# Kernel tuning notes

Hardware: AMD Instinct MI355X
Metric: run time of the kernel (lower is better)

Reference implementation:

```python
import jax, jax.numpy as jnp
import numpy as np

NEG = 1e12  # matches torch code's -1e12 masking constant


def _rope_sincos(seq_len, dim, dtype):
    # SinusoidalPositionEmbedding with merge_mode='zero':
    # emb[n, i] pairs -> reshape to [n, dim] as [sin0, cos0, sin1, cos1, ...]
    pos = jnp.arange(seq_len, dtype=jnp.float32)
    inv = jnp.power(10000.0, -2.0 * jnp.arange(dim // 2, dtype=jnp.float32) / dim)
    ang = pos[:, None] * inv[None, :]            # [n, d/2]
    sin, cos = jnp.sin(ang), jnp.cos(ang)
    # cos_pos = pos[..., 1::2].repeat_interleave(2) == repeat(cos, 2)
    cos_pos = jnp.repeat(cos, 2, axis=-1).astype(dtype)  # [n, d]
    sin_pos = jnp.repeat(sin, 2, axis=-1).astype(dtype)  # [n, d]
    return sin_pos, cos_pos


def _rotate_half(x):
    # stack([-x[..., 1::2], x[..., ::2]], -1).reshape(x.shape)
    x2 = jnp.stack([-x[..., 1::2], x[..., ::2]], axis=-1)
    return x2.reshape(x.shape)


def setup_inputs() -> dict:
    key = jax.random.key(0)
    k1, k2, k3 = jax.random.split(key, 3)
    B, N, H = 8, 1024, 768
    heads, head_size = 12, 64
    inputs = jax.random.normal(k1, (B, N, H), dtype=jnp.float32)
    mask = jnp.ones((B, N), dtype=jnp.float32)
    W = jax.random.normal(k2, (H, heads * head_size * 2), dtype=jnp.float32) * (H ** -0.5)
    b = jnp.zeros((heads * head_size * 2,), dtype=jnp.float32)
    return {"inputs": inputs, "mask": mask, "W": W, "b": b}


def reference(inputs, mask, W, b):
    heads, head_size = 12, 64
    B, N, _ = inputs.shape
    x = inputs @ W + b                              # [B, N, heads*head_size*2]
    x = x.reshape(B, N, heads, 2 * head_size)       # split+stack over heads
    qw, kw = x[..., :head_size], x[..., head_size:]  # [B, N, heads, d]

    sin_pos, cos_pos = _rope_sincos(N, head_size, inputs.dtype)
    sin_pos = sin_pos[None, :, None, :]             # [1, N, 1, d]
    cos_pos = cos_pos[None, :, None, :]
    qw = qw * cos_pos + _rotate_half(qw) * sin_pos
    kw = kw * cos_pos + _rotate_half(kw) * sin_pos

    logits = jnp.einsum('bmhd,bnhd->bhmn', qw, kw)  # [B, heads, N, N]

    m1 = mask[:, None, :, None]                     # mask rows (axis ndim-2)
    m2 = mask[:, None, None, :]                     # mask cols (axis ndim-1)
    logits = logits * m1 + (-NEG) * (1.0 - m1)
    logits = logits * m2 + (-NEG) * (1.0 - m2)
    tril = jnp.tril(jnp.ones((N, N), dtype=logits.dtype), k=-1)
    logits = logits - tril * NEG                    # forbid end < start
    return logits / (head_size ** 0.5)
```

## Files before the change

### kernel.cpp

```cpp
#include <hip/hip_runtime.h>
#include <stdint.h>

#define NEGC 1000000000000.0f

using f32x4  = __attribute__((ext_vector_type(4))) float;
using short8 = __attribute__((ext_vector_type(8))) short;

typedef __attribute__((address_space(3))) uint32_t* lds_ptr_t;
typedef const __attribute__((address_space(1))) uint32_t* gptr_t;

__device__ __forceinline__ void gload_lds16(const void* g, const void* l) {
  __builtin_amdgcn_global_load_lds((gptr_t)g, (lds_ptr_t)l, 16, 0, 0);
}

__device__ __forceinline__ unsigned short f2bf(float f) {
  union { float f; uint32_t u; } v; v.f = f;
  uint32_t u = v.u;
  return (unsigned short)((u + 0x7fffu + ((u >> 16) & 1u)) >> 16);
}

__global__ void k_sincos(float* __restrict__ s, float* __restrict__ c) {
  int idx = blockIdx.x * 256 + threadIdx.x;
  int m = idx >> 5, i = idx & 31;
  float inv = expf(-(float)i * (9.210340371976184f / 32.0f));
  float ang = (float)m * inv;
  s[idx] = sinf(ang);
  c[idx] = cosf(ang);
}

__global__ void k_cvt(const float* __restrict__ in, unsigned short* __restrict__ out, int n4) {
  int idx = blockIdx.x * blockDim.x + threadIdx.x;
  if (idx < n4) {
    float4 v = ((const float4*)in)[idx];
    ushort4 o;
    o.x = f2bf(v.x); o.y = f2bf(v.y); o.z = f2bf(v.z); o.w = f2bf(v.w);
    ((ushort4*)out)[idx] = o;
  }
}

__global__ void k_transW(const float* __restrict__ W, unsigned short* __restrict__ Wt) {
  __shared__ float tile[64][65];
  int kb = blockIdx.x;
  int nb = blockIdx.y;
  int t = threadIdx.x;
  int c = t & 63, r0 = t >> 6;
#pragma unroll
  for (int p = 0; p < 16; ++p) {
    int r = r0 + p * 4;
    tile[r][c] = W[(size_t)(kb * 64 + r) * 1536 + nb * 64 + c];
  }
  __syncthreads();
#pragma unroll
  for (int p = 0; p < 16; ++p) {
    int n = r0 + p * 4;
    Wt[(size_t)(nb * 64 + n) * 768 + kb * 64 + c] = f2bf(tile[c][n]);
  }
}

__global__ __launch_bounds__(256) void k_gemm1(
    const unsigned short* __restrict__ A,
    const unsigned short* __restrict__ Bt,
    const float* __restrict__ bias,
    const float* __restrict__ ssin, const float* __restrict__ scos,
    unsigned short* __restrict__ qb, unsigned short* __restrict__ kb) {
  __shared__ __align__(16) unsigned short As[128 * 64];
  __shared__ __align__(16) unsigned short Bs[128 * 64];
  const int tid = threadIdx.x;
  const int wave = tid >> 6, lane = tid & 63;
  const int wm = wave >> 1, wn = wave & 1;
  const int m0 = blockIdx.x * 128;
  const int h  = blockIdx.y;
  const int j0 = h * 128;
  const int lr = lane >> 3, kc = lane & 7;

  f32x4 acc[4][4] = {};

  for (int kt = 0; kt < 12; ++kt) {
    const int k0 = kt * 64;
#pragma unroll
    for (int i = 0; i < 4; ++i) {
      int row = i * 32 + wave * 8 + lr;
      int gk = k0 + ((kc ^ (row & 7)) << 3);
      gload_lds16(&A[(size_t)(m0 + row) * 768 + gk], &As[(i * 32 + wave * 8) * 64]);
    }
#pragma unroll
    for (int i = 0; i < 4; ++i) {
      int row = i * 32 + wave * 8 + lr;
      int gk = k0 + ((kc ^ (row & 7)) << 3);
      gload_lds16(&Bt[(size_t)(j0 + row) * 768 + gk], &Bs[(i * 32 + wave * 8) * 64]);
    }
    asm volatile("s_waitcnt vmcnt(0)" ::: "memory");
    __syncthreads();
#pragma unroll
    for (int kh = 0; kh < 2; ++kh) {
      short8 af[4], bfr[4];
#pragma unroll
      for (int mt = 0; mt < 4; ++mt) {
        int row = wm * 64 + mt * 16 + (lane & 15);
        int cs = (kh * 4 + (lane >> 4)) ^ (row & 7);
        af[mt] = *(const short8*)&As[row * 64 + cs * 8];
      }
#pragma unroll
      for (int nt = 0; nt < 4; ++nt) {
        int row = wn * 64 + nt * 16 + (lane & 15);
        int cs = (kh * 4 + (lane >> 4)) ^ (row & 7);
        bfr[nt] = *(const short8*)&Bs[row * 64 + cs * 8];
      }
#pragma unroll
      for (int mt = 0; mt < 4; ++mt)
#pragma unroll
        for (int nt = 0; nt < 4; ++nt)
          acc[mt][nt] = __builtin_amdgcn_mfma_f32_16x16x32_bf16(af[mt], bfr[nt], acc[mt][nt], 0, 0, 0);
    }
    __syncthreads();
  }

  const int col = lane & 15, rquad = lane >> 4;
  unsigned short* dst = (wn == 0) ? qb : kb;
#pragma unroll
  for (int nt = 0; nt < 4; ++nt) {
    const int d = nt * 16 + col;
    const float bv = bias[j0 + wn * 64 + d];
    const int ifr = d >> 1;
    const float sgn = (d & 1) ? 1.0f : -1.0f;
#pragma unroll
    for (int mt = 0; mt < 4; ++mt) {
#pragma unroll
      for (int j = 0; j < 4; ++j) {
        int mg = m0 + wm * 64 + mt * 16 + rquad * 4 + j;
        int ms = mg & 1023, bi = mg >> 10;
        float v = acc[mt][nt][j] + bv;
        float p = __shfl_xor(v, 1, 64);
        float s = ssin[ms * 32 + ifr], cv = scos[ms * 32 + ifr];
        float r = v * cv + sgn * p * s;
        dst[(size_t)((bi * 12 + h) * 1024 + ms) * 64 + d] = f2bf(r);
      }
    }
  }
}

__global__ __launch_bounds__(256) void k_gemm2(
    const unsigned short* __restrict__ qb, const unsigned short* __restrict__ kbuf,
    const float* __restrict__ mask, float* __restrict__ out) {
  __shared__ __align__(16) unsigned short Qs[128 * 64];
  __shared__ __align__(16) unsigned short Ks[128 * 64];
  const int tid = threadIdx.x;
  const int wave = tid >> 6, lane = tid & 63;
  const int wm = wave >> 1, wn = wave & 1;
  const int bh = blockIdx.y;
  const int tm = blockIdx.x >> 3, tn = blockIdx.x & 7;
  const int b = bh / 12;
  const int lr = lane >> 3, kc = lane & 7;

  const unsigned short* qbase = qb   + (size_t)bh * (1024 * 64);
  const unsigned short* kbase = kbuf + (size_t)bh * (1024 * 64);

#pragma unroll
  for (int i = 0; i < 4; ++i) {
    int row = i * 32 + wave * 8 + lr;
    int gk = (kc ^ (row & 7)) << 3;
    gload_lds16(&qbase[(size_t)(tm * 128 + row) * 64 + gk], &Qs[(i * 32 + wave * 8) * 64]);
  }
#pragma unroll
  for (int i = 0; i < 4; ++i) {
    int row = i * 32 + wave * 8 + lr;
    int gk = (kc ^ (row & 7)) << 3;
    gload_lds16(&kbase[(size_t)(tn * 128 + row) * 64 + gk], &Ks[(i * 32 + wave * 8) * 64]);
  }
  asm volatile("s_waitcnt vmcnt(0)" ::: "memory");
  __syncthreads();

  f32x4 acc[4][4] = {};
#pragma unroll
  for (int kh = 0; kh < 2; ++kh) {
    short8 af[4], bfr[4];
#pragma unroll
    for (int mt = 0; mt < 4; ++mt) {
      int row = wm * 64 + mt * 16 + (lane & 15);
      int cs = (kh * 4 + (lane >> 4)) ^ (row & 7);
      af[mt] = *(const short8*)&Qs[row * 64 + cs * 8];
    }
#pragma unroll
    for (int nt = 0; nt < 4; ++nt) {
      int row = wn * 64 + nt * 16 + (lane & 15);
      int cs = (kh * 4 + (lane >> 4)) ^ (row & 7);
      bfr[nt] = *(const short8*)&Ks[row * 64 + cs * 8];
    }
#pragma unroll
    for (int mt = 0; mt < 4; ++mt)
#pragma unroll
      for (int nt = 0; nt < 4; ++nt)
        acc[mt][nt] = __builtin_amdgcn_mfma_f32_16x16x32_bf16(af[mt], bfr[nt], acc[mt][nt], 0, 0, 0);
  }

  float* obase = out + (size_t)bh * (1024 * 1024);
  const int col = lane & 15, rquad = lane >> 4;
  float m2v[4]; int ngv[4];
#pragma unroll
  for (int nt = 0; nt < 4; ++nt) {
    ngv[nt] = tn * 128 + wn * 64 + nt * 16 + col;
    m2v[nt] = mask[b * 1024 + ngv[nt]];
  }
#pragma unroll
  for (int mt = 0; mt < 4; ++mt) {
#pragma unroll
    for (int j = 0; j < 4; ++j) {
      int mg = tm * 128 + wm * 64 + mt * 16 + rquad * 4 + j;
      float m1 = mask[b * 1024 + mg];
      float* orow = obase + (size_t)mg * 1024;
#pragma unroll
      for (int nt = 0; nt < 4; ++nt) {
        float v = acc[mt][nt][j];
        v = v * m1 - NEGC * (1.0f - m1);
        v = v * m2v[nt] - NEGC * (1.0f - m2v[nt]);
        if (ngv[nt] < mg) v -= NEGC;
        orow[ngv[nt]] = v * 0.125f;
      }
    }
  }
}

extern "C" void kernel_launch(void* const* d_in, const int* in_sizes, int n_in,
                              void* d_out, int out_size, void* d_ws, size_t ws_size,
                              hipStream_t stream) {
  const float* inputs = (const float*)d_in[0];
  const float* mask   = (const float*)d_in[1];
  const float* W      = (const float*)d_in[2];
  const float* bias   = (const float*)d_in[3];
  float* out = (float*)d_out;
  char* ws = (char*)d_ws;

  float* ssin = (float*)(ws);
  float* scos = (float*)(ws + 131072);
  unsigned short* inA = (unsigned short*)(ws + 262144);
  unsigned short* Wt  = (unsigned short*)(ws + 262144 + 12582912);
  unsigned short* qb  = (unsigned short*)(ws + 262144 + 12582912 + 2359296);
  unsigned short* kb  = (unsigned short*)(ws + 262144 + 12582912 + 2359296 + 12582912);

  hipLaunchKernelGGL(k_sincos, dim3(128), dim3(256), 0, stream, ssin, scos);
  hipLaunchKernelGGL(k_cvt, dim3(6144), dim3(256), 0, stream, inputs, inA, 1572864);
  hipLaunchKernelGGL(k_transW, dim3(12, 24), dim3(256), 0, stream, W, Wt);
  hipLaunchKernelGGL(k_gemm1, dim3(64, 12), dim3(256), 0, stream,
                     inA, Wt, bias, ssin, scos, qb, kb);
  hipLaunchKernelGGL(k_gemm2, dim3(64, 96), dim3(256), 0, stream, qb, kb, mask, out);
}
```

Before: 140.2 us.

## Fuse prep kernels into one launch and remap GEMM blocks for XCD locality

Merges the bf16 input conversion, the W transpose and the sin/cos table kernels into a single launch that branches on block index. This removes two launches and their inter-kernel gaps. Both GEMM kernels now use a 1D grid whose block index is remapped so that blocks dispatched to the same XCD share M-tiles (gemm1) or batch-head slices (gemm2), aiming for better L2 reuse per XCD. The remapping assumes round-robin dispatch of blocks across 8 XCDs. The fused prep kernel also allocates the transpose tile in shared memory for every block, including those that never use it.

```diff
diff --git a/kernel.cpp b/kernel.cpp
--- a/kernel.cpp
+++ b/kernel.cpp
@@ -19,41 +19,40 @@
   return (unsigned short)((u + 0x7fffu + ((u >> 16) & 1u)) >> 16);
 }
 
-__global__ void k_sincos(float* __restrict__ s, float* __restrict__ c) {
-  int idx = blockIdx.x * 256 + threadIdx.x;
-  int m = idx >> 5, i = idx & 31;
-  float inv = expf(-(float)i * (9.210340371976184f / 32.0f));
-  float ang = (float)m * inv;
-  s[idx] = sinf(ang);
-  c[idx] = cosf(ang);
-}
-
-__global__ void k_cvt(const float* __restrict__ in, unsigned short* __restrict__ out, int n4) {
-  int idx = blockIdx.x * blockDim.x + threadIdx.x;
-  if (idx < n4) {
+__global__ __launch_bounds__(256) void k_prep(
+    const float* __restrict__ in, unsigned short* __restrict__ inb,
+    const float* __restrict__ W, unsigned short* __restrict__ Wt,
+    float* __restrict__ ssin, float* __restrict__ scos) {
+  __shared__ float tile[64][65];
+  const int bx = blockIdx.x, t = threadIdx.x;
+  if (bx < 6144) {
+    int idx = bx * 256 + t;
     float4 v = ((const float4*)in)[idx];
     ushort4 o;
     o.x = f2bf(v.x); o.y = f2bf(v.y); o.z = f2bf(v.z); o.w = f2bf(v.w);
-    ((ushort4*)out)[idx] = o;
-  }
-}
-
-__global__ void k_transW(const float* __restrict__ W, unsigned short* __restrict__ Wt) {
-  __shared__ float tile[64][65];
-  int kb = blockIdx.x;
-  int nb = blockIdx.y;
-  int t = threadIdx.x;
-  int c = t & 63, r0 = t >> 6;
-#pragma unroll
-  for (int p = 0; p < 16; ++p) {
-    int r = r0 + p * 4;
-    tile[r][c] = W[(size_t)(kb * 64 + r) * 1536 + nb * 64 + c];
-  }
-  __syncthreads();
-#pragma unroll
-  for (int p = 0; p < 16; ++p) {
-    int n = r0 + p * 4;
-    Wt[(size_t)(nb * 64 + n) * 768 + kb * 64 + c] = f2bf(tile[c][n]);
+    ((ushort4*)inb)[idx] = o;
+  } else if (bx < 6432) {
+    int b = bx - 6144;
+    int kb = b % 12, nb = b / 12;
+    int c = t & 63, r0 = t >> 6;
+#pragma unroll
+    for (int p = 0; p < 16; ++p) {
+      int r = r0 + p * 4;
+      tile[r][c] = W[(size_t)(kb * 64 + r) * 1536 + nb * 64 + c];
+    }
+    __syncthreads();
+#pragma unroll
+    for (int p = 0; p < 16; ++p) {
+      int n = r0 + p * 4;
+      Wt[(size_t)(nb * 64 + n) * 768 + kb * 64 + c] = f2bf(tile[c][n]);
+    }
+  } else {
+    int idx = (bx - 6432) * 256 + t;
+    int m = idx >> 5, i = idx & 31;
+    float inv = expf(-(float)i * (9.210340371976184f / 32.0f));
+    float ang = (float)m * inv;
+    ssin[idx] = sinf(ang);
+    scos[idx] = cosf(ang);
   }
 }
 
@@ -68,9 +67,12 @@
   const int tid = threadIdx.x;
   const int wave = tid >> 6, lane = tid & 63;
   const int wm = wave >> 1, wn = wave & 1;
-  const int m0 = blockIdx.x * 128;
-  const int h  = blockIdx.y;
-  const int j0 = h * 128;
+  const int orig = blockIdx.x;
+  const int xcd = orig & 7, idx = orig >> 3;
+  const int mt8 = idx / 12;
+  const int h   = idx - mt8 * 12;
+  const int m0  = (xcd * 8 + mt8) * 128;
+  const int j0  = h * 128;
   const int lr = lane >> 3, kc = lane & 7;
 
   f32x4 acc[4][4] = {};
@@ -147,8 +149,11 @@
   const int tid = threadIdx.x;
   const int wave = tid >> 6, lane = tid & 63;
   const int wm = wave >> 1, wn = wave & 1;
-  const int bh = blockIdx.y;
-  const int tm = blockIdx.x >> 3, tn = blockIdx.x & 7;
+  const int orig = blockIdx.x;
+  const int xcd = orig & 7, idx = orig >> 3;
+  const int bh = xcd * 12 + (idx >> 6);
+  const int tt = idx & 63;
+  const int tm = tt >> 3, tn = tt & 7;
   const int b = bh / 12;
   const int lr = lane >> 3, kc = lane & 7;
 
@@ -237,10 +242,9 @@
   unsigned short* qb  = (unsigned short*)(ws + 262144 + 12582912 + 2359296);
   unsigned short* kb  = (unsigned short*)(ws + 262144 + 12582912 + 2359296 + 12582912);
 
-  hipLaunchKernelGGL(k_sincos, dim3(128), dim3(256), 0, stream, ssin, scos);
-  hipLaunchKernelGGL(k_cvt, dim3(6144), dim3(256), 0, stream, inputs, inA, 1572864);
-  hipLaunchKernelGGL(k_transW, dim3(12, 24), dim3(256), 0, stream, W, Wt);
-  hipLaunchKernelGGL(k_gemm1, dim3(64, 12), dim3(256), 0, stream,
+  hipLaunchKernelGGL(k_prep, dim3(6560), dim3(256), 0, stream,
+                     inputs, inA, W, Wt, ssin, scos);
+  hipLaunchKernelGGL(k_gemm1, dim3(768), dim3(256), 0, stream,
                      inA, Wt, bias, ssin, scos, qb, kb);
-  hipLaunchKernelGGL(k_gemm2, dim3(64, 96), dim3(256), 0, stream, qb, kb, mask, out);
-}
+  hipLaunchKernelGGL(k_gemm2, dim3(6144), dim3(256), 0, stream, qb, kb, mask, out);
+}
```

Result: faster. 130.8 us (-6.7%).
